# Performance work log

Measured on AMD Instinct MI355X. Metric: run time of the kernel, lower is better.

Reference implementation:

```python
import jax, jax.numpy as jnp
import numpy as np


def setup_inputs() -> dict:
    key = jax.random.key(0)
    k1, k2 = jax.random.split(key)
    B, T, J, D = 32, 2048, 64, 256
    h = jax.random.normal(k1, (B, T, D), dtype=jnp.float32)
    s = jax.random.normal(k2, (B, T, J), dtype=jnp.float32)
    return {"h": h, "s": s}


def reference(h, s):
    # z1: max similarity over query positions -> [B, T]
    z1 = jnp.max(s, axis=-1)
    # attention over context positions -> [B, T]
    b = jax.nn.softmax(z1, axis=-1)
    # weighted sum of context vectors -> [B, D]
    pooled = jnp.einsum('bt,btd->bd', b, h)
    # tile pooled vector across all T context positions -> [B, T, D]
    q2c = jnp.broadcast_to(pooled[:, None, :], h.shape)
    return q2c
```

## Files before the change

### kernel.cpp

```cpp
#include <hip/hip_runtime.h>
#include <math.h>

#define BQ 32
#define TQ 2048
#define JQ 64
#define DQ 256
#define NBLK1 2048
#define NBLK2 1024
#define NTHR 256

typedef float f4 __attribute__((ext_vector_type(4)));


__global__ __launch_bounds__(NTHR) void k_fused_pool(
    const f4* __restrict__ s4, const f4* __restrict__ h4,
    float* __restrict__ dpart, float* __restrict__ ppart)
{
    const int blk = blockIdx.x, tid = threadIdx.x;
    const int b = blk >> 6;
    const int t0 = (blk & 63) * 32;
    __shared__ float e_lds[32];

    #pragma unroll
    for (int p = 0; p < 2; ++p) {
        int idx = blk * 512 + p * 256 + tid;
        f4 v = __builtin_nontemporal_load(&s4[idx]);
        float m = fmaxf(fmaxf(v.x, v.y), fmaxf(v.z, v.w));
        m = fmaxf(m, __shfl_xor(m, 1));
        m = fmaxf(m, __shfl_xor(m, 2));
        m = fmaxf(m, __shfl_xor(m, 4));
        m = fmaxf(m, __shfl_xor(m, 8));
        if ((tid & 15) == 0)
            e_lds[p * 16 + (tid >> 4)] = expf(m);
    }
    __syncthreads();

    if (tid < 32) {
        float v = e_lds[tid];
        v += __shfl_xor(v, 16);
        v += __shfl_xor(v, 8);
        v += __shfl_xor(v, 4);
        v += __shfl_xor(v, 2);
        v += __shfl_xor(v, 1);
        if (tid == 0) dpart[blk] = v;
    }

    const int t_sub = tid >> 6;
    const int d4 = tid & 63;
    f4 acc = (f4)(0.f);
    #pragma unroll
    for (int i = 0; i < 8; ++i) {
        int tl = i * 4 + t_sub;
        float wt = e_lds[tl];
        f4 hv = __builtin_nontemporal_load(
            &h4[(size_t)(b * TQ + t0 + tl) * (DQ / 4) + d4]);
        acc += wt * hv;
    }

    __shared__ float sred[NTHR][4];
    sred[tid][0] = acc.x; sred[tid][1] = acc.y;
    sred[tid][2] = acc.z; sred[tid][3] = acc.w;
    __syncthreads();
    int dd4 = tid >> 2, c4 = tid & 3;
    float sum = sred[dd4][c4] + sred[64 + dd4][c4] +
                sred[128 + dd4][c4] + sred[192 + dd4][c4];
    ppart[blk * DQ + tid] = sum;
}

__global__ __launch_bounds__(NTHR) void k_reduce_bcast(
    const float* __restrict__ dpart, const float* __restrict__ ppart,
    f4* __restrict__ out4)
{
    const int blk = blockIdx.x, tid = threadIdx.x;
    const int b = blk >> 5;
    __shared__ __align__(16) float pooled[DQ];

    float den = 0.f;
    #pragma unroll
    for (int c = 0; c < 64; ++c)
        den += dpart[b * 64 + c];
    const float inv = 1.0f / den;

    float p = 0.f;
    #pragma unroll
    for (int c = 0; c < 64; ++c)
        p += ppart[(b * 64 + c) * DQ + tid];
    pooled[tid] = p * inv;
    __syncthreads();

    f4 pv = ((const f4*)pooled)[tid & 63];
    size_t base = (size_t)blk * 4096;
    #pragma unroll
    for (int k = 0; k < 16; ++k)
        __builtin_nontemporal_store(pv, &out4[base + k * 256 + tid]);
}

extern "C" void kernel_launch(void* const* d_in, const int* in_sizes, int n_in,
                              void* d_out, int out_size, void* d_ws, size_t ws_size,
                              hipStream_t stream) {
    const f4* h4 = (const f4*)d_in[0];
    const f4* s4 = (const f4*)d_in[1];
    f4* out4 = (f4*)d_out;

    float* ws = (float*)d_ws;
    float* dpart = ws;
    float* ppart = ws + NBLK1;

    k_fused_pool<<<NBLK1, NTHR, 0, stream>>>(s4, h4, dpart, ppart);
    k_reduce_bcast<<<NBLK2, NTHR, 0, stream>>>(dpart, ppart, out4);
}
```

Measured before the change: 127.0 us.

## Keep softmax weights in registers per wave and vectorize partial-sum reduction

In the pooling kernel each wave now owns 8 contiguous time steps, so its exp weights stay in registers and are fetched by lane shuffles instead of going through shared memory. This removes one block-wide barrier, and the denominator is reduced within the wave before being combined through a small shared array. In the broadcast kernel the 64-way reduction over partials uses float4 loads split across the four waves and is finished in shared memory, cutting the serial load chain per thread. It adds a few more shuffles in exchange.

```diff
diff --git a/kernel.cpp b/kernel.cpp
--- a/kernel.cpp
+++ b/kernel.cpp
@@ -19,61 +19,57 @@
     const int blk = blockIdx.x, tid = threadIdx.x;
     const int b = blk >> 6;
     const int t0 = (blk & 63) * 32;
-    __shared__ float e_lds[32];
+    const int w = tid >> 6;
+    const int lane = tid & 63;
 
+    float e[2];
     #pragma unroll
     for (int p = 0; p < 2; ++p) {
-        int idx = blk * 512 + p * 256 + tid;
+        int idx = blk * 512 + w * 128 + p * 64 + lane;
         f4 v = __builtin_nontemporal_load(&s4[idx]);
         float m = fmaxf(fmaxf(v.x, v.y), fmaxf(v.z, v.w));
         m = fmaxf(m, __shfl_xor(m, 1));
         m = fmaxf(m, __shfl_xor(m, 2));
         m = fmaxf(m, __shfl_xor(m, 4));
         m = fmaxf(m, __shfl_xor(m, 8));
-        if ((tid & 15) == 0)
-            e_lds[p * 16 + (tid >> 4)] = expf(m);
+        e[p] = expf(m);
     }
-    __syncthreads();
+    float dw = e[0] + e[1];
+    dw += __shfl_xor(dw, 16);
+    dw += __shfl_xor(dw, 32);
 
-    if (tid < 32) {
-        float v = e_lds[tid];
-        v += __shfl_xor(v, 16);
-        v += __shfl_xor(v, 8);
-        v += __shfl_xor(v, 4);
-        v += __shfl_xor(v, 2);
-        v += __shfl_xor(v, 1);
-        if (tid == 0) dpart[blk] = v;
-    }
-
-    const int t_sub = tid >> 6;
-    const int d4 = tid & 63;
     f4 acc = (f4)(0.f);
     #pragma unroll
-    for (int i = 0; i < 8; ++i) {
-        int tl = i * 4 + t_sub;
-        float wt = e_lds[tl];
+    for (int j = 0; j < 8; ++j) {
+        float wt = __shfl(e[j >> 2], (j & 3) << 4);
+        int tl = w * 8 + j;
         f4 hv = __builtin_nontemporal_load(
-            &h4[(size_t)(b * TQ + t0 + tl) * (DQ / 4) + d4]);
+            &h4[(size_t)(b * TQ + t0 + tl) * (DQ / 4) + lane]);
         acc += wt * hv;
     }
 
     __shared__ float sred[NTHR][4];
+    __shared__ float dred[4];
     sred[tid][0] = acc.x; sred[tid][1] = acc.y;
     sred[tid][2] = acc.z; sred[tid][3] = acc.w;
+    if (lane == 0) dred[w] = dw;
     __syncthreads();
     int dd4 = tid >> 2, c4 = tid & 3;
     float sum = sred[dd4][c4] + sred[64 + dd4][c4] +
                 sred[128 + dd4][c4] + sred[192 + dd4][c4];
     ppart[blk * DQ + tid] = sum;
+    if (tid == 0)
+        dpart[blk] = (dred[0] + dred[1]) + (dred[2] + dred[3]);
 }
 
 __global__ __launch_bounds__(NTHR) void k_reduce_bcast(
-    const float* __restrict__ dpart, const float* __restrict__ ppart,
+    const float* __restrict__ dpart, const f4* __restrict__ ppart4,
     f4* __restrict__ out4)
 {
     const int blk = blockIdx.x, tid = threadIdx.x;
     const int b = blk >> 5;
-    __shared__ __align__(16) float pooled[DQ];
+    const int w = tid >> 6, lane = tid & 63;
+    __shared__ __align__(16) f4 pp[NTHR];
 
     float den = 0.f;
     #pragma unroll
@@ -81,14 +77,17 @@
         den += dpart[b * 64 + c];
     const float inv = 1.0f / den;
 
-    float p = 0.f;
+    f4 p = (f4)(0.f);
     #pragma unroll
-    for (int c = 0; c < 64; ++c)
-        p += ppart[(b * 64 + c) * DQ + tid];
-    pooled[tid] = p * inv;
+    for (int k = 0; k < 16; ++k) {
+        int c = k * 4 + w;
+        p += ppart4[(size_t)(b * 64 + c) * (DQ / 4) + lane];
+    }
+    pp[tid] = p;
     __syncthreads();
+    f4 pv = (pp[lane] + pp[64 + lane]) + (pp[128 + lane] + pp[192 + lane]);
+    pv *= inv;
 
-    f4 pv = ((const f4*)pooled)[tid & 63];
     size_t base = (size_t)blk * 4096;
     #pragma unroll
     for (int k = 0; k < 16; ++k)
@@ -107,5 +106,5 @@
     float* ppart = ws + NBLK1;
 
     k_fused_pool<<<NBLK1, NTHR, 0, stream>>>(s4, h4, dpart, ppart);
-    k_reduce_bcast<<<NBLK2, NTHR, 0, stream>>>(dpart, ppart, out4);
+    k_reduce_bcast<<<NBLK2, NTHR, 0, stream>>>(dpart, (const f4*)ppart, out4);
 }
```

After: 126.6 us. No clear change (-0.3%).
